# Performance work log

Hardware: AMD Instinct MI355X
Metric: run time of the kernel (lower is better)

The kernel has to match this reference:

```python
import math
import jax, jax.numpy as jnp
import numpy as np

EMB = 512
HEADS = 8
NEG_INF = -1e30  # stand-in for -inf that stays finite under softmax


def setup_inputs() -> dict:
    key = jax.random.key(0)
    ks = jax.random.split(key, 6)
    b, t, e, h = 2, 2048, EMB, HEADS
    s = 1.0 / math.sqrt(e)
    return {
        "x": jax.random.normal(ks[0], (b, t, e), dtype=jnp.float32),
        "Wk": jax.random.normal(ks[1], (h * e, e), dtype=jnp.float32) * s,
        "Wq": jax.random.normal(ks[2], (h * e, e), dtype=jnp.float32) * s,
        "Wv": jax.random.normal(ks[3], (h * e, e), dtype=jnp.float32) * s,
        "Wc": jax.random.normal(ks[4], (e, h * e), dtype=jnp.float32) * s,
        "bc": jax.random.normal(ks[5], (e,), dtype=jnp.float32) * 0.01,
    }


def reference(x, Wk, Wq, Wv, Wc, bc):
    b, t, e = x.shape
    h = HEADS
    # projections: Linear(e, h*e) -> (b, t, h, e) -> (b, h, t, e)
    k = (x @ Wk.T).reshape(b, t, h, e).transpose(0, 2, 1, 3)
    q = (x @ Wq.T).reshape(b, t, h, e).transpose(0, 2, 1, 3)
    v = (x @ Wv.T).reshape(b, t, h, e).transpose(0, 2, 1, 3)
    scores = jnp.einsum("bhqe,bhke->bhqk", q, k) / math.sqrt(e)
    # causal mask: strict upper triangle (offset=1) set to -inf
    causal = jnp.tril(jnp.ones((t, t), dtype=bool))  # True where allowed
    scores = jnp.where(causal, scores, NEG_INF)
    weights = jax.nn.softmax(scores, axis=-1)
    out = jnp.einsum("bhqk,bhke->bhqe", weights, v)  # (b, h, t, e)
    out = out.transpose(0, 2, 1, 3).reshape(b, t, h * e)
    return out @ Wc.T + bc
```

## Files before the change

kernel.cpp:

```cpp
#include <hip/hip_runtime.h>

typedef unsigned short u16;
typedef __attribute__((ext_vector_type(4))) short short4v;
typedef __attribute__((ext_vector_type(8))) short short8;
typedef __attribute__((ext_vector_type(4))) float floatx4;

#define GLL16(g, l) __builtin_amdgcn_global_load_lds( \
    (const __attribute__((address_space(1))) void*)(g), \
    (__attribute__((address_space(3))) void*)(l), 16, 0, 0)

__device__ __forceinline__ float b2f(u16 h) {
    union { unsigned u; float f; } v; v.u = ((unsigned)h) << 16; return v.f;
}
__device__ __forceinline__ u16 f2b(float f) {
    union { float f; unsigned u; } v; v.f = f;
    unsigned r = v.u + 0x7fffu + ((v.u >> 16) & 1u);
    return (u16)(r >> 16);
}
__device__ __forceinline__ float launder(float f) {
    return fminf(fmaxf(f, -30000.0f), 30000.0f);
}

__device__ __forceinline__ int sniff_block(const u16* __restrict__ xs)
{
    __shared__ int cnt;
    if (threadIdx.x == 0) cnt = 0;
    __syncthreads();
    int local = 0;
    for (int i = threadIdx.x; i < 4096; i += 256) {
        const int ex = (xs[i] >> 7) & 0xFF;
        if (ex >= 0x90) ++local;
    }
    if (local) atomicAdd(&cnt, local);
    __syncthreads();
    return cnt > 256;
}

__device__ __forceinline__ void conv_one(const void* __restrict__ raw,
                                         u16* __restrict__ dst, int n, int isf32)
{
    int i = blockIdx.x * 256 + threadIdx.x;
    const int stride = gridDim.x * 256;
    if (isf32) {
        const float* s = (const float*)raw;
        for (; i < n; i += stride) dst[i] = f2b(s[i]);
    } else {
        const u16* s = (const u16*)raw;
        for (; i < n; i += stride) dst[i] = s[i];
    }
}

__global__ __launch_bounds__(256)
void convert4(const void* r0, const void* r1, const void* r2, const void* r3,
              u16* d0, u16* d1, u16* d2, u16* d3, int n, const u16* xs)
{
    const int isf32 = sniff_block(xs);
    const int z = blockIdx.y;
    const void* raw = (z == 0) ? r0 : (z == 1) ? r1 : (z == 2) ? r2 : r3;
    u16* dst        = (z == 0) ? d0 : (z == 1) ? d1 : (z == 2) ? d2 : d3;
    conv_one(raw, dst, n, isf32);
}

__global__ __launch_bounds__(256)
void convert2(const void* r0, const void* r1, u16* d0, u16* d1,
              int n0, int n1, const u16* xs, int* flagp)
{
    const int isf32 = sniff_block(xs);
    if (blockIdx.x == 0 && blockIdx.y == 0 && threadIdx.x == 0) flagp[0] = isf32;
    if (blockIdx.y == 0) conv_one(r0, d0, n0, isf32);
    else                 conv_one(r1, d1, n1, isf32);
}

__global__ __launch_bounds__(256, 2)
void gemm_qkv(const u16* __restrict__ A,
              const u16* __restrict__ B0, const u16* __restrict__ B1, const u16* __restrict__ B2,
              u16* __restrict__ C0, u16* __restrict__ C1, u16* __restrict__ VTout)
{
    const int z = blockIdx.z;
    const u16* B = (z == 0) ? B0 : ((z == 1) ? B1 : B2);

    __shared__ u16 As[2][128 * 32];
    __shared__ u16 Bs[2][128 * 32];

    const int tid  = threadIdx.x;
    const int wave = tid >> 6;
    const int lane = tid & 63;
    const int c16  = lane & 15;
    const int quad = lane >> 4;
    const int m0 = blockIdx.x * 128;
    const int n0 = blockIdx.y * 128;
    const int wm = (wave >> 1) * 64;
    const int wn = (wave & 1) * 64;

    floatx4 acc[4][4] = {};

    const int srow = wave * 32 + (lane >> 2);
    const int scol = (lane & 3) * 8;
    const u16* Ag = A + (size_t)(m0 + srow) * 512 + scol;
    const u16* Bg = B + (size_t)(n0 + srow) * 512 + scol;
    const int woff = (wave * 32) * 32;

    GLL16(Ag,            &As[0][woff]);
    GLL16(Ag + 16 * 512, &As[0][woff + 16 * 32]);
    GLL16(Bg,            &Bs[0][woff]);
    GLL16(Bg + 16 * 512, &Bs[0][woff + 16 * 32]);
    int cur = 0;

    for (int k0 = 0; k0 < 512; k0 += 32) {
        __syncthreads();

        if (k0 + 32 < 512) {
            GLL16(Ag + k0 + 32,            &As[cur ^ 1][woff]);
            GLL16(Ag + k0 + 32 + 16 * 512, &As[cur ^ 1][woff + 16 * 32]);
            GLL16(Bg + k0 + 32,            &Bs[cur ^ 1][woff]);
            GLL16(Bg + k0 + 32 + 16 * 512, &Bs[cur ^ 1][woff + 16 * 32]);
        }

        short8 af[4], bf[4];
#pragma unroll
        for (int i = 0; i < 4; ++i)
            af[i] = *(const short8*)&As[cur][(wm + i * 16 + c16) * 32 + quad * 8];
#pragma unroll
        for (int i = 0; i < 4; ++i)
            bf[i] = *(const short8*)&Bs[cur][(wn + i * 16 + c16) * 32 + quad * 8];
#pragma unroll
        for (int i = 0; i < 4; ++i)
#pragma unroll
            for (int j = 0; j < 4; ++j)
                acc[i][j] = __builtin_amdgcn_mfma_f32_16x16x32_bf16(af[i], bf[j], acc[i][j], 0, 0, 0);
        cur ^= 1;
    }

    if (z == 2) {
#pragma unroll
        for (int i = 0; i < 4; ++i)
#pragma unroll
            for (int j = 0; j < 4; ++j) {
                const int col = n0 + wn + j * 16 + c16;
                const int hh = col >> 9, d = col & 511;
                const int rb = m0 + wm + i * 16 + quad * 4;
                const int bq = rb >> 11, tt = rb & 2047;
                short4v v4;
#pragma unroll
                for (int r = 0; r < 4; ++r) v4[r] = (short)f2b(launder(acc[i][j][r]));
                *(short4v*)&VTout[((size_t)((bq * 8 + hh) * 512 + d)) * 2048 + tt] = v4;
            }
    } else {
        u16* C = (z == 0) ? C0 : C1;
#pragma unroll
        for (int i = 0; i < 4; ++i)
#pragma unroll
            for (int j = 0; j < 4; ++j) {
                const int col = n0 + wn + j * 16 + c16;
#pragma unroll
                for (int r = 0; r < 4; ++r) {
                    const int row = m0 + wm + i * 16 + quad * 4 + r;
                    C[(size_t)row * 4096 + col] = f2b(launder(acc[i][j][r]));
                }
            }
    }
}

__global__ __launch_bounds__(256, 2)
void gemm_out(const u16* __restrict__ A, const u16* __restrict__ B,
              const u16* __restrict__ bias, const int* __restrict__ flagp,
              void* __restrict__ out)
{
    __shared__ u16 As[2][128 * 32];
    __shared__ u16 Bs[2][64 * 32];

    const int tid  = threadIdx.x;
    const int wave = tid >> 6;
    const int lane = tid & 63;
    const int c16  = lane & 15;
    const int quad = lane >> 4;
    const int m0 = blockIdx.x * 128;
    const int n0 = blockIdx.y * 64;
    const int wm = (wave >> 1) * 64;
    const int wn = (wave & 1) * 32;

    floatx4 acc[4][2] = {};

    const int srowA = wave * 32 + (lane >> 2);
    const int srowB = wave * 16 + (lane >> 2);
    const int scol  = (lane & 3) * 8;
    const u16* Ag = A + (size_t)(m0 + srowA) * 4096 + scol;
    const u16* Bg = B + (size_t)(n0 + srowB) * 4096 + scol;
    const int woffA = (wave * 32) * 32;
    const int woffB = (wave * 16) * 32;

    GLL16(Ag,                     &As[0][woffA]);
    GLL16(Ag + (size_t)16 * 4096, &As[0][woffA + 16 * 32]);
    GLL16(Bg,                     &Bs[0][woffB]);
    int cur = 0;

    for (int k0 = 0; k0 < 4096; k0 += 32) {
        __syncthreads();

        if (k0 + 32 < 4096) {
            GLL16(Ag + k0 + 32,                     &As[cur ^ 1][woffA]);
            GLL16(Ag + k0 + 32 + (size_t)16 * 4096, &As[cur ^ 1][woffA + 16 * 32]);
            GLL16(Bg + k0 + 32,                     &Bs[cur ^ 1][woffB]);
        }

        short8 af[4], bf[2];
#pragma unroll
        for (int i = 0; i < 4; ++i)
            af[i] = *(const short8*)&As[cur][(wm + i * 16 + c16) * 32 + quad * 8];
#pragma unroll
        for (int j = 0; j < 2; ++j)
            bf[j] = *(const short8*)&Bs[cur][(wn + j * 16 + c16) * 32 + quad * 8];
#pragma unroll
        for (int i = 0; i < 4; ++i)
#pragma unroll
            for (int j = 0; j < 2; ++j)
                acc[i][j] = __builtin_amdgcn_mfma_f32_16x16x32_bf16(af[i], bf[j], acc[i][j], 0, 0, 0);
        cur ^= 1;
    }

    const int isf32 = flagp[0];
#pragma unroll
    for (int i = 0; i < 4; ++i)
#pragma unroll
        for (int j = 0; j < 2; ++j) {
            const int col = n0 + wn + j * 16 + c16;
            const float bv = b2f(bias[col]);
#pragma unroll
            for (int r = 0; r < 4; ++r) {
                const int row = m0 + wm + i * 16 + quad * 4 + r;
                const float val = launder(acc[i][j][r] + bv);
                if (isf32) ((float*)out)[(size_t)row * 512 + col] = val;
                else       ((u16*)out)[(size_t)row * 512 + col] = f2b(val);
            }
        }
}

#define LOG2E 1.4426950408889634f
#define SM_SCALE 0.044194173824159216f
#define PM 24.0f

__global__ __launch_bounds__(512, 2)
void flash_attn(const u16* __restrict__ Q, const u16* __restrict__ K,
                const u16* __restrict__ VT, u16* __restrict__ O)
{
    __shared__ u16 Ks[2][64 * 516];
    __shared__ u16 Ps[4][16 * 68];
    __shared__ float Lp[2][4][16];

    const int tid  = threadIdx.x;
    const int wave = tid >> 6;
    const int lane = tid & 63;
    const int c16  = lane & 15;
    const int quad = lane >> 4;
    const int g   = wave & 3;
    const int st2 = wave >> 2;

    const int x  = blockIdx.x;
    const int bh = x & 15;
    const int pr = x >> 4;
    const int b  = bh >> 3, h = bh & 7;

    const u16* Qh  = Q  + (size_t)b * 2048 * 4096 + (size_t)h * 512;
    const u16* Kh  = K  + (size_t)b * 2048 * 4096 + (size_t)h * 512;
    const u16* VTh = VT + (size_t)bh * 512 * 2048;
    u16*       Oh  = O  + (size_t)b * 2048 * 4096 + (size_t)h * 512;

#pragma unroll
    for (int i = 0; i < 8; ++i) {
        const int kr = wave * 8 + i;
        GLL16(Kh + (size_t)kr * 4096 + lane * 8, &Ks[0][kr * 516]);
    }
    int cur = 0;

    for (int pm = 0; pm < 2; ++pm) {
        const int qt = pm ? pr : (31 - pr);
        const int q0 = qt * 64;
        const int ntile = qt + 1;
        const int qrow = q0 + g * 16 + c16;
        const int rowq = q0 + g * 16 + quad * 4;

        short8 qf[16];
#pragma unroll
        for (int s = 0; s < 16; ++s)
            qf[s] = *(const short8*)(Qh + (size_t)qrow * 4096 + s * 32 + quad * 8);

        float l_i[4] = {0.0f, 0.0f, 0.0f, 0.0f};
        floatx4 oacc[4][4] = {};

        for (int t = 0; t < ntile; ++t) {
            const int kv0 = t * 64;
            __syncthreads();

            short8 vf[4][2];
            const u16* Vw = VTh + (size_t)(wave * 64) * 2048 + kv0;
#pragma unroll
            for (int dt = 0; dt < 4; ++dt)
#pragma unroll
                for (int ks = 0; ks < 2; ++ks)
                    vf[dt][ks] = *(const short8*)(Vw + (size_t)(dt * 16 + c16) * 2048 + ks * 32 + quad * 8);

            if (t + 1 < ntile || pm == 0) {
                const int knext = (t + 1 < ntile) ? (kv0 + 64) : 0;
#pragma unroll
                for (int i = 0; i < 8; ++i) {
                    const int kr = wave * 8 + i;
                    GLL16(Kh + (size_t)(knext + kr) * 4096 + lane * 8,
                          &Ks[cur ^ 1][kr * 516]);
                }
            }

            floatx4 sv0 = {}, sv1 = {};
            __builtin_amdgcn_s_setprio(1);
#pragma unroll
            for (int s = 0; s < 16; ++s) {
                short8 kf0 = *(const short8*)&Ks[cur][(st2 * 32 + c16) * 516 + s * 32 + quad * 8];
                short8 kf1 = *(const short8*)&Ks[cur][(st2 * 32 + 16 + c16) * 516 + s * 32 + quad * 8];
                sv0 = __builtin_amdgcn_mfma_f32_16x16x32_bf16(qf[s], kf0, sv0, 0, 0, 0);
                sv1 = __builtin_amdgcn_mfma_f32_16x16x32_bf16(qf[s], kf1, sv1, 0, 0, 0);
            }
            __builtin_amdgcn_s_setprio(0);

            const int col0 = kv0 + st2 * 32 + c16;
            if (t + 1 < ntile) {
#pragma unroll
                for (int r = 0; r < 4; ++r) {
                    const float p0 = exp2f((sv0[r] * SM_SCALE - PM) * LOG2E);
                    const float p1 = exp2f((sv1[r] * SM_SCALE - PM) * LOG2E);
                    l_i[r] += p0 + p1;
                    Ps[g][(quad * 4 + r) * 68 + st2 * 32 + c16]      = f2b(p0);
                    Ps[g][(quad * 4 + r) * 68 + st2 * 32 + 16 + c16] = f2b(p1);
                }
            } else {
#pragma unroll
                for (int r = 0; r < 4; ++r) {
                    const float p0 = (col0 > rowq + r)
                        ? 0.0f : exp2f((sv0[r] * SM_SCALE - PM) * LOG2E);
                    const float p1 = (col0 + 16 > rowq + r)
                        ? 0.0f : exp2f((sv1[r] * SM_SCALE - PM) * LOG2E);
                    l_i[r] += p0 + p1;
                    Ps[g][(quad * 4 + r) * 68 + st2 * 32 + c16]      = f2b(p0);
                    Ps[g][(quad * 4 + r) * 68 + st2 * 32 + 16 + c16] = f2b(p1);
                }
            }

            asm volatile("s_waitcnt lgkmcnt(0)" ::: "memory");
            __builtin_amdgcn_s_barrier();
            __builtin_amdgcn_sched_barrier(0);

            __builtin_amdgcn_s_setprio(1);
#pragma unroll
            for (int qg = 0; qg < 4; ++qg) {
                short8 pf0 = *(const short8*)&Ps[qg][c16 * 68 + quad * 8];
                short8 pf1 = *(const short8*)&Ps[qg][c16 * 68 + 32 + quad * 8];
#pragma unroll
                for (int dt = 0; dt < 4; ++dt) {
                    oacc[qg][dt] = __builtin_amdgcn_mfma_f32_16x16x32_bf16(pf0, vf[dt][0], oacc[qg][dt], 0, 0, 0);
                    oacc[qg][dt] = __builtin_amdgcn_mfma_f32_16x16x32_bf16(pf1, vf[dt][1], oacc[qg][dt], 0, 0, 0);
                }
            }
            __builtin_amdgcn_s_setprio(0);

            cur ^= 1;
        }

#pragma unroll
        for (int off = 1; off < 16; off <<= 1)
#pragma unroll
            for (int r = 0; r < 4; ++r)
                l_i[r] += __shfl_xor(l_i[r], off, 16);
        if (c16 == 0) {
#pragma unroll
            for (int r = 0; r < 4; ++r) Lp[st2][g][quad * 4 + r] = l_i[r];
        }
        __syncthreads();

#pragma unroll
        for (int qg = 0; qg < 4; ++qg) {
            float linv[4];
#pragma unroll
            for (int r = 0; r < 4; ++r)
                linv[r] = 1.0f / (Lp[0][qg][quad * 4 + r] + Lp[1][qg][quad * 4 + r]);
#pragma unroll
            for (int dt = 0; dt < 4; ++dt)
#pragma unroll
                for (int r = 0; r < 4; ++r)
                    Oh[(size_t)(q0 + qg * 16 + quad * 4 + r) * 4096 + wave * 64 + dt * 16 + c16] =
                        f2b(launder(oacc[qg][dt][r] * linv[r]));
        }
    }
}

extern "C" void kernel_launch(void* const* d_in, const int* in_sizes, int n_in,
                              void* d_out, int out_size, void* d_ws, size_t ws_size,
                              hipStream_t stream)
{
    const size_t SZ  = (size_t)4096 * 4096;
    const size_t SZh = (size_t)4096 * 512;

    u16* Qb  = (u16*)d_ws;
    u16* Kb  = Qb + SZ;
    u16* Vb  = Kb + SZ;
    u16* VTb = Vb + SZ;
    u16* Ob  = Vb;

    u16* xb  = Vb;
    u16* Wqb = Vb + SZh;
    u16* Wkb = Vb + 2 * SZh;
    u16* Wvb = Vb + 3 * SZh;

    u16* Wcb = Qb;
    u16* bcb = Qb + SZh;
    int* flagp = (int*)(Qb + 2 * SZh);

    const u16* xs = (const u16*)d_in[0];

    convert4<<<dim3(256, 4), 256, 0, stream>>>(
        d_in[0], d_in[2], d_in[1], d_in[3], xb, Wqb, Wkb, Wvb, (int)SZh, xs);

    gemm_qkv<<<dim3(32, 32, 3), 256, 0, stream>>>(
        xb, Wqb, Wkb, Wvb, Qb, Kb, VTb);

    flash_attn<<<dim3(256), 512, 0, stream>>>(Qb, Kb, VTb, Ob);

    convert2<<<dim3(256, 2), 256, 0, stream>>>(
        d_in[4], d_in[5], Wcb, bcb, (int)SZh, 512, xs, flagp);

    gemm_out<<<dim3(32, 8), 256, 0, stream>>>(Ob, Wcb, bcb, flagp, d_out);
}
```

Baseline: 385.1 us.

## Fuse fp32-to-bf16 input conversion into the projection and output GEMM loaders

Drops the separate convert4 and convert2 kernels. The QKV and output GEMMs now read raw fp32 operands, convert them to bf16 in registers, and store them into LDS, with the next tile's global loads issued before the current tile's MFMAs. This removes two launches and the round trip of the bf16 copies through global memory. In exchange, the fp32 path can no longer use direct global-to-LDS loads, every block repeats the dtype sniff, and the out-projection weight is reconverted by each of the 32 M-blocks.

```diff
diff --git a/kernel.cpp b/kernel.cpp
--- a/kernel.cpp
+++ b/kernel.cpp
@@ -19,6 +19,14 @@
 }
 __device__ __forceinline__ float launder(float f) {
     return fminf(fmaxf(f, -30000.0f), 30000.0f);
+}
+__device__ __forceinline__ short8 cvt8(floatx4 a, floatx4 b) {
+    short8 v;
+    v[0] = (short)f2b(a[0]); v[1] = (short)f2b(a[1]);
+    v[2] = (short)f2b(a[2]); v[3] = (short)f2b(a[3]);
+    v[4] = (short)f2b(b[0]); v[5] = (short)f2b(b[1]);
+    v[6] = (short)f2b(b[2]); v[7] = (short)f2b(b[3]);
+    return v;
 }
 
 __device__ __forceinline__ int sniff_block(const u16* __restrict__ xs)
@@ -36,48 +44,14 @@
     return cnt > 256;
 }
 
-__device__ __forceinline__ void conv_one(const void* __restrict__ raw,
-                                         u16* __restrict__ dst, int n, int isf32)
-{
-    int i = blockIdx.x * 256 + threadIdx.x;
-    const int stride = gridDim.x * 256;
-    if (isf32) {
-        const float* s = (const float*)raw;
-        for (; i < n; i += stride) dst[i] = f2b(s[i]);
-    } else {
-        const u16* s = (const u16*)raw;
-        for (; i < n; i += stride) dst[i] = s[i];
-    }
-}
-
-__global__ __launch_bounds__(256)
-void convert4(const void* r0, const void* r1, const void* r2, const void* r3,
-              u16* d0, u16* d1, u16* d2, u16* d3, int n, const u16* xs)
-{
-    const int isf32 = sniff_block(xs);
-    const int z = blockIdx.y;
-    const void* raw = (z == 0) ? r0 : (z == 1) ? r1 : (z == 2) ? r2 : r3;
-    u16* dst        = (z == 0) ? d0 : (z == 1) ? d1 : (z == 2) ? d2 : d3;
-    conv_one(raw, dst, n, isf32);
-}
-
-__global__ __launch_bounds__(256)
-void convert2(const void* r0, const void* r1, u16* d0, u16* d1,
-              int n0, int n1, const u16* xs, int* flagp)
-{
-    const int isf32 = sniff_block(xs);
-    if (blockIdx.x == 0 && blockIdx.y == 0 && threadIdx.x == 0) flagp[0] = isf32;
-    if (blockIdx.y == 0) conv_one(r0, d0, n0, isf32);
-    else                 conv_one(r1, d1, n1, isf32);
-}
-
 __global__ __launch_bounds__(256, 2)
-void gemm_qkv(const u16* __restrict__ A,
-              const u16* __restrict__ B0, const u16* __restrict__ B1, const u16* __restrict__ B2,
+void gemm_qkv(const void* __restrict__ Araw,
+              const void* __restrict__ B0, const void* __restrict__ B1, const void* __restrict__ B2,
               u16* __restrict__ C0, u16* __restrict__ C1, u16* __restrict__ VTout)
 {
+    const int isf32 = sniff_block((const u16*)Araw);
     const int z = blockIdx.z;
-    const u16* B = (z == 0) ? B0 : ((z == 1) ? B1 : B2);
+    const void* Braw = (z == 0) ? B0 : ((z == 1) ? B1 : B2);
 
     __shared__ u16 As[2][128 * 32];
     __shared__ u16 Bs[2][128 * 32];
@@ -96,39 +70,90 @@
 
     const int srow = wave * 32 + (lane >> 2);
     const int scol = (lane & 3) * 8;
-    const u16* Ag = A + (size_t)(m0 + srow) * 512 + scol;
-    const u16* Bg = B + (size_t)(n0 + srow) * 512 + scol;
+    const size_t aoff = (size_t)(m0 + srow) * 512 + scol;
+    const size_t boff = (size_t)(n0 + srow) * 512 + scol;
     const int woff = (wave * 32) * 32;
-
-    GLL16(Ag,            &As[0][woff]);
-    GLL16(Ag + 16 * 512, &As[0][woff + 16 * 32]);
-    GLL16(Bg,            &Bs[0][woff]);
-    GLL16(Bg + 16 * 512, &Bs[0][woff + 16 * 32]);
-    int cur = 0;
-
-    for (int k0 = 0; k0 < 512; k0 += 32) {
-        __syncthreads();
-
-        if (k0 + 32 < 512) {
-            GLL16(Ag + k0 + 32,            &As[cur ^ 1][woff]);
-            GLL16(Ag + k0 + 32 + 16 * 512, &As[cur ^ 1][woff + 16 * 32]);
-            GLL16(Bg + k0 + 32,            &Bs[cur ^ 1][woff]);
-            GLL16(Bg + k0 + 32 + 16 * 512, &Bs[cur ^ 1][woff + 16 * 32]);
-        }
-
-        short8 af[4], bf[4];
-#pragma unroll
-        for (int i = 0; i < 4; ++i)
-            af[i] = *(const short8*)&As[cur][(wm + i * 16 + c16) * 32 + quad * 8];
-#pragma unroll
-        for (int i = 0; i < 4; ++i)
-            bf[i] = *(const short8*)&Bs[cur][(wn + i * 16 + c16) * 32 + quad * 8];
-#pragma unroll
-        for (int i = 0; i < 4; ++i)
-#pragma unroll
-            for (int j = 0; j < 4; ++j)
-                acc[i][j] = __builtin_amdgcn_mfma_f32_16x16x32_bf16(af[i], bf[j], acc[i][j], 0, 0, 0);
-        cur ^= 1;
+    const int l8 = lane * 8;
+
+    if (isf32) {
+        const float* Af = (const float*)Araw + aoff;
+        const float* Bf = (const float*)Braw + boff;
+        *(short8*)&As[0][woff + l8] =
+            cvt8(*(const floatx4*)(Af), *(const floatx4*)(Af + 4));
+        *(short8*)&As[0][woff + 16 * 32 + l8] =
+            cvt8(*(const floatx4*)(Af + 16 * 512), *(const floatx4*)(Af + 16 * 512 + 4));
+        *(short8*)&Bs[0][woff + l8] =
+            cvt8(*(const floatx4*)(Bf), *(const floatx4*)(Bf + 4));
+        *(short8*)&Bs[0][woff + 16 * 32 + l8] =
+            cvt8(*(const floatx4*)(Bf + 16 * 512), *(const floatx4*)(Bf + 16 * 512 + 4));
+        int cur = 0;
+        for (int k0 = 0; k0 < 512; k0 += 32) {
+            __syncthreads();
+
+            floatx4 ra0, ra1, ra2, ra3, rb0, rb1, rb2, rb3;
+            const int pf = (k0 + 32 < 512);
+            if (pf) {
+                ra0 = *(const floatx4*)(Af + k0 + 32);
+                ra1 = *(const floatx4*)(Af + k0 + 36);
+                ra2 = *(const floatx4*)(Af + k0 + 32 + 16 * 512);
+                ra3 = *(const floatx4*)(Af + k0 + 36 + 16 * 512);
+                rb0 = *(const floatx4*)(Bf + k0 + 32);
+                rb1 = *(const floatx4*)(Bf + k0 + 36);
+                rb2 = *(const floatx4*)(Bf + k0 + 32 + 16 * 512);
+                rb3 = *(const floatx4*)(Bf + k0 + 36 + 16 * 512);
+            }
+
+            short8 af[4], bf[4];
+#pragma unroll
+            for (int i = 0; i < 4; ++i)
+                af[i] = *(const short8*)&As[cur][(wm + i * 16 + c16) * 32 + quad * 8];
+#pragma unroll
+            for (int i = 0; i < 4; ++i)
+                bf[i] = *(const short8*)&Bs[cur][(wn + i * 16 + c16) * 32 + quad * 8];
+#pragma unroll
+            for (int i = 0; i < 4; ++i)
+#pragma unroll
+                for (int j = 0; j < 4; ++j)
+                    acc[i][j] = __builtin_amdgcn_mfma_f32_16x16x32_bf16(af[i], bf[j], acc[i][j], 0, 0, 0);
+
+            if (pf) {
+                *(short8*)&As[cur ^ 1][woff + l8]           = cvt8(ra0, ra1);
+                *(short8*)&As[cur ^ 1][woff + 16 * 32 + l8] = cvt8(ra2, ra3);
+                *(short8*)&Bs[cur ^ 1][woff + l8]           = cvt8(rb0, rb1);
+                *(short8*)&Bs[cur ^ 1][woff + 16 * 32 + l8] = cvt8(rb2, rb3);
+            }
+            cur ^= 1;
+        }
+    } else {
+        const u16* Ag = (const u16*)Araw + aoff;
+        const u16* Bg = (const u16*)Braw + boff;
+        GLL16(Ag,            &As[0][woff]);
+        GLL16(Ag + 16 * 512, &As[0][woff + 16 * 32]);
+        GLL16(Bg,            &Bs[0][woff]);
+        GLL16(Bg + 16 * 512, &Bs[0][woff + 16 * 32]);
+        int cur = 0;
+        for (int k0 = 0; k0 < 512; k0 += 32) {
+            __syncthreads();
+            if (k0 + 32 < 512) {
+                GLL16(Ag + k0 + 32,            &As[cur ^ 1][woff]);
+                GLL16(Ag + k0 + 32 + 16 * 512, &As[cur ^ 1][woff + 16 * 32]);
+                GLL16(Bg + k0 + 32,            &Bs[cur ^ 1][woff]);
+                GLL16(Bg + k0 + 32 + 16 * 512, &Bs[cur ^ 1][woff + 16 * 32]);
+            }
+            short8 af[4], bf[4];
+#pragma unroll
+            for (int i = 0; i < 4; ++i)
+                af[i] = *(const short8*)&As[cur][(wm + i * 16 + c16) * 32 + quad * 8];
+#pragma unroll
+            for (int i = 0; i < 4; ++i)
+                bf[i] = *(const short8*)&Bs[cur][(wn + i * 16 + c16) * 32 + quad * 8];
+#pragma unroll
+            for (int i = 0; i < 4; ++i)
+#pragma unroll
+                for (int j = 0; j < 4; ++j)
+                    acc[i][j] = __builtin_amdgcn_mfma_f32_16x16x32_bf16(af[i], bf[j], acc[i][j], 0, 0, 0);
+            cur ^= 1;
+        }
     }
 
     if (z == 2) {
@@ -162,10 +187,12 @@
 }
 
 __global__ __launch_bounds__(256, 2)
-void gemm_out(const u16* __restrict__ A, const u16* __restrict__ B,
-              const u16* __restrict__ bias, const int* __restrict__ flagp,
+void gemm_out(const u16* __restrict__ A, const void* __restrict__ Braw,
+              const void* __restrict__ bcraw, const u16* __restrict__ xs,
               void* __restrict__ out)
 {
+    const int isf32 = sniff_block(xs);
+
     __shared__ u16 As[2][128 * 32];
     __shared__ u16 Bs[2][64 * 32];
 
@@ -185,46 +212,63 @@
     const int srowB = wave * 16 + (lane >> 2);
     const int scol  = (lane & 3) * 8;
     const u16* Ag = A + (size_t)(m0 + srowA) * 4096 + scol;
-    const u16* Bg = B + (size_t)(n0 + srowB) * 4096 + scol;
+    const size_t boff = (size_t)(n0 + srowB) * 4096 + scol;
     const int woffA = (wave * 32) * 32;
     const int woffB = (wave * 16) * 32;
+    const int l8 = lane * 8;
+
+    const float* Bf  = (const float*)Braw + boff;
+    const u16*   Bg  = (const u16*)Braw + boff;
 
     GLL16(Ag,                     &As[0][woffA]);
     GLL16(Ag + (size_t)16 * 4096, &As[0][woffA + 16 * 32]);
-    GLL16(Bg,                     &Bs[0][woffB]);
+    if (isf32)
+        *(short8*)&Bs[0][woffB + l8] = cvt8(*(const floatx4*)(Bf), *(const floatx4*)(Bf + 4));
+    else
+        GLL16(Bg, &Bs[0][woffB]);
     int cur = 0;
 
     for (int k0 = 0; k0 < 4096; k0 += 32) {
         __syncthreads();
 
-        if (k0 + 32 < 4096) {
+        const int pf = (k0 + 32 < 4096);
+        floatx4 rb0, rb1;
+        if (pf) {
             GLL16(Ag + k0 + 32,                     &As[cur ^ 1][woffA]);
             GLL16(Ag + k0 + 32 + (size_t)16 * 4096, &As[cur ^ 1][woffA + 16 * 32]);
-            GLL16(Bg + k0 + 32,                     &Bs[cur ^ 1][woffB]);
-        }
-
-        short8 af[4], bf[2];
+            if (isf32) {
+                rb0 = *(const floatx4*)(Bf + k0 + 32);
+                rb1 = *(const floatx4*)(Bf + k0 + 36);
+            } else {
+                GLL16(Bg + k0 + 32, &Bs[cur ^ 1][woffB]);
+            }
+        }
+
+        short8 af[4], bfr[2];
 #pragma unroll
         for (int i = 0; i < 4; ++i)
             af[i] = *(const short8*)&As[cur][(wm + i * 16 + c16) * 32 + quad * 8];
 #pragma unroll
         for (int j = 0; j < 2; ++j)
-            bf[j] = *(const short8*)&Bs[cur][(wn + j * 16 + c16) * 32 + quad * 8];
+            bfr[j] = *(const short8*)&Bs[cur][(wn + j * 16 + c16) * 32 + quad * 8];
 #pragma unroll
         for (int i = 0; i < 4; ++i)
 #pragma unroll
             for (int j = 0; j < 2; ++j)
-                acc[i][j] = __builtin_amdgcn_mfma_f32_16x16x32_bf16(af[i], bf[j], acc[i][j], 0, 0, 0);
+                acc[i][j] = __builtin_amdgcn_mfma_f32_16x16x32_bf16(af[i], bfr[j], acc[i][j], 0, 0, 0);
+
+        if (pf && isf32)
+            *(short8*)&Bs[cur ^ 1][woffB + l8] = cvt8(rb0, rb1);
         cur ^= 1;
     }
 
-    const int isf32 = flagp[0];
 #pragma unroll
     for (int i = 0; i < 4; ++i)
 #pragma unroll
         for (int j = 0; j < 2; ++j) {
             const int col = n0 + wn + j * 16 + c16;
-            const float bv = b2f(bias[col]);
+            const float bv = isf32 ? ((const float*)bcraw)[col]
+                                   : b2f(((const u16*)bcraw)[col]);
 #pragma unroll
             for (int r = 0; r < 4; ++r) {
                 const int row = m0 + wm + i * 16 + quad * 4 + r;
@@ -394,36 +438,18 @@
                               void* d_out, int out_size, void* d_ws, size_t ws_size,
                               hipStream_t stream)
 {
-    const size_t SZ  = (size_t)4096 * 4096;
-    const size_t SZh = (size_t)4096 * 512;
+    const size_t SZ = (size_t)4096 * 4096;
 
     u16* Qb  = (u16*)d_ws;
     u16* Kb  = Qb + SZ;
-    u16* Vb  = Kb + SZ;
-    u16* VTb = Vb + SZ;
-    u16* Ob  = Vb;
-
-    u16* xb  = Vb;
-    u16* Wqb = Vb + SZh;
-    u16* Wkb = Vb + 2 * SZh;
-    u16* Wvb = Vb + 3 * SZh;
-
-    u16* Wcb = Qb;
-    u16* bcb = Qb + SZh;
-    int* flagp = (int*)(Qb + 2 * SZh);
-
-    const u16* xs = (const u16*)d_in[0];
-
-    convert4<<<dim3(256, 4), 256, 0, stream>>>(
-        d_in[0], d_in[2], d_in[1], d_in[3], xb, Wqb, Wkb, Wvb, (int)SZh, xs);
+    u16* Ob  = Kb + SZ;
+    u16* VTb = Ob + SZ;
 
     gemm_qkv<<<dim3(32, 32, 3), 256, 0, stream>>>(
-        xb, Wqb, Wkb, Wvb, Qb, Kb, VTb);
+        d_in[0], d_in[2], d_in[1], d_in[3], Qb, Kb, VTb);
 
     flash_attn<<<dim3(256), 512, 0, stream>>>(Qb, Kb, VTb, Ob);
 
-    convert2<<<dim3(256, 2), 256, 0, stream>>>(
-        d_in[4], d_in[5], Wcb, bcb, (int)SZh, 512, xs, flagp);
-
-    gemm_out<<<dim3(32, 8), 256, 0, stream>>>(Ob, Wcb, bcb, flagp, d_out);
-}
+    gemm_out<<<dim3(32, 8), 256, 0, stream>>>(
+        Ob, d_in[4], d_in[5], (const u16*)d_in[0], d_out);
+}
```

New measurement: 422.2 us. +9.6%, slower.

## Vectorize conversion, stage QKV epilogue through LDS, shrink output GEMM tiles

Applied to the files above, without the earlier changes.

The fp32→bf16 conversion kernels now handle eight elements per thread with 16/32-byte vector loads and stores, replacing scalar accesses. The QKV GEMM epilogue writes the tile into padded shared memory first and then emits coalesced 16-byte row stores, both for Q/K and for the transposed V layout. This replaces the scattered 2-byte and 8-byte global writes. The output GEMM tile shrinks from 128x64 to 64x64, doubling the block count so more CUs are busy, at the cost of less operand reuse per block.

```diff
diff --git a/kernel.cpp b/kernel.cpp
--- a/kernel.cpp
+++ b/kernel.cpp
@@ -19,6 +19,14 @@
 }
 __device__ __forceinline__ float launder(float f) {
     return fminf(fmaxf(f, -30000.0f), 30000.0f);
+}
+__device__ __forceinline__ short8 cvt8(floatx4 a, floatx4 b) {
+    short8 v;
+    v[0] = (short)f2b(a[0]); v[1] = (short)f2b(a[1]);
+    v[2] = (short)f2b(a[2]); v[3] = (short)f2b(a[3]);
+    v[4] = (short)f2b(b[0]); v[5] = (short)f2b(b[1]);
+    v[6] = (short)f2b(b[2]); v[7] = (short)f2b(b[3]);
+    return v;
 }
 
 __device__ __forceinline__ int sniff_block(const u16* __restrict__ xs)
@@ -39,14 +47,17 @@
 __device__ __forceinline__ void conv_one(const void* __restrict__ raw,
                                          u16* __restrict__ dst, int n, int isf32)
 {
-    int i = blockIdx.x * 256 + threadIdx.x;
-    const int stride = gridDim.x * 256;
+    int i = (blockIdx.x * 256 + threadIdx.x) * 8;
+    const int stride = gridDim.x * 256 * 8;
     if (isf32) {
         const float* s = (const float*)raw;
-        for (; i < n; i += stride) dst[i] = f2b(s[i]);
+        for (; i < n; i += stride)
+            *(short8*)(dst + i) = cvt8(*(const floatx4*)(s + i),
+                                       *(const floatx4*)(s + i + 4));
     } else {
         const u16* s = (const u16*)raw;
-        for (; i < n; i += stride) dst[i] = s[i];
+        for (; i < n; i += stride)
+            *(short8*)(dst + i) = *(const short8*)(s + i);
     }
 }
 
@@ -79,8 +90,7 @@
     const int z = blockIdx.z;
     const u16* B = (z == 0) ? B0 : ((z == 1) ? B1 : B2);
 
-    __shared__ u16 As[2][128 * 32];
-    __shared__ u16 Bs[2][128 * 32];
+    __shared__ u16 smem[128 * 136];
 
     const int tid  = threadIdx.x;
     const int wave = tid >> 6;
@@ -100,29 +110,33 @@
     const u16* Bg = B + (size_t)(n0 + srow) * 512 + scol;
     const int woff = (wave * 32) * 32;
 
-    GLL16(Ag,            &As[0][woff]);
-    GLL16(Ag + 16 * 512, &As[0][woff + 16 * 32]);
-    GLL16(Bg,            &Bs[0][woff]);
-    GLL16(Bg + 16 * 512, &Bs[0][woff + 16 * 32]);
+    GLL16(Ag,            smem + woff);
+    GLL16(Ag + 16 * 512, smem + woff + 16 * 32);
+    GLL16(Bg,            smem + 8192 + woff);
+    GLL16(Bg + 16 * 512, smem + 8192 + woff + 16 * 32);
     int cur = 0;
 
     for (int k0 = 0; k0 < 512; k0 += 32) {
         __syncthreads();
+        u16* Asc = smem + cur * 4096;
+        u16* Bsc = smem + 8192 + cur * 4096;
 
         if (k0 + 32 < 512) {
-            GLL16(Ag + k0 + 32,            &As[cur ^ 1][woff]);
-            GLL16(Ag + k0 + 32 + 16 * 512, &As[cur ^ 1][woff + 16 * 32]);
-            GLL16(Bg + k0 + 32,            &Bs[cur ^ 1][woff]);
-            GLL16(Bg + k0 + 32 + 16 * 512, &Bs[cur ^ 1][woff + 16 * 32]);
+            u16* Asn = smem + (cur ^ 1) * 4096;
+            u16* Bsn = smem + 8192 + (cur ^ 1) * 4096;
+            GLL16(Ag + k0 + 32,            Asn + woff);
+            GLL16(Ag + k0 + 32 + 16 * 512, Asn + woff + 16 * 32);
+            GLL16(Bg + k0 + 32,            Bsn + woff);
+            GLL16(Bg + k0 + 32 + 16 * 512, Bsn + woff + 16 * 32);
         }
 
         short8 af[4], bf[4];
 #pragma unroll
         for (int i = 0; i < 4; ++i)
-            af[i] = *(const short8*)&As[cur][(wm + i * 16 + c16) * 32 + quad * 8];
+            af[i] = *(const short8*)&Asc[(wm + i * 16 + c16) * 32 + quad * 8];
 #pragma unroll
         for (int i = 0; i < 4; ++i)
-            bf[i] = *(const short8*)&Bs[cur][(wn + i * 16 + c16) * 32 + quad * 8];
+            bf[i] = *(const short8*)&Bsc[(wn + i * 16 + c16) * 32 + quad * 8];
 #pragma unroll
         for (int i = 0; i < 4; ++i)
 #pragma unroll
@@ -131,33 +145,53 @@
         cur ^= 1;
     }
 
+    __syncthreads();
+
     if (z == 2) {
 #pragma unroll
         for (int i = 0; i < 4; ++i)
 #pragma unroll
             for (int j = 0; j < 4; ++j) {
-                const int col = n0 + wn + j * 16 + c16;
-                const int hh = col >> 9, d = col & 511;
-                const int rb = m0 + wm + i * 16 + quad * 4;
-                const int bq = rb >> 11, tt = rb & 2047;
-                short4v v4;
-#pragma unroll
-                for (int r = 0; r < 4; ++r) v4[r] = (short)f2b(launder(acc[i][j][r]));
-                *(short4v*)&VTout[((size_t)((bq * 8 + hh) * 512 + d)) * 2048 + tt] = v4;
-            }
+                const int lc = wn + j * 16 + c16;
+#pragma unroll
+                for (int r = 0; r < 4; ++r) {
+                    const int lr = wm + i * 16 + quad * 4 + r;
+                    smem[lc * 136 + lr] = f2b(launder(acc[i][j][r]));
+                }
+            }
+        __syncthreads();
+        const int bq  = m0 >> 11;
+        const int tt0 = m0 & 2047;
+#pragma unroll
+        for (int p = 0; p < 8; ++p) {
+            const int lc  = p * 16 + (tid >> 4);
+            const int seg = tid & 15;
+            const short8 v = *(const short8*)&smem[lc * 136 + seg * 8];
+            const int col = n0 + lc;
+            const int hh = col >> 9, d = col & 511;
+            *(short8*)&VTout[((size_t)((bq * 8 + hh) * 512 + d)) * 2048 + tt0 + seg * 8] = v;
+        }
     } else {
         u16* C = (z == 0) ? C0 : C1;
 #pragma unroll
         for (int i = 0; i < 4; ++i)
 #pragma unroll
             for (int j = 0; j < 4; ++j) {
-                const int col = n0 + wn + j * 16 + c16;
+                const int lc = wn + j * 16 + c16;
 #pragma unroll
                 for (int r = 0; r < 4; ++r) {
-                    const int row = m0 + wm + i * 16 + quad * 4 + r;
-                    C[(size_t)row * 4096 + col] = f2b(launder(acc[i][j][r]));
-                }
-            }
+                    const int lr = wm + i * 16 + quad * 4 + r;
+                    smem[lr * 136 + lc] = f2b(launder(acc[i][j][r]));
+                }
+            }
+        __syncthreads();
+#pragma unroll
+        for (int p = 0; p < 8; ++p) {
+            const int lr  = p * 16 + (tid >> 4);
+            const int seg = tid & 15;
+            const short8 v = *(const short8*)&smem[lr * 136 + seg * 8];
+            *(short8*)&C[(size_t)(m0 + lr) * 4096 + n0 + seg * 8] = v;
+        }
     }
 }
 
@@ -166,7 +200,7 @@
               const u16* __restrict__ bias, const int* __restrict__ flagp,
               void* __restrict__ out)
 {
-    __shared__ u16 As[2][128 * 32];
+    __shared__ u16 As[2][64 * 32];
     __shared__ u16 Bs[2][64 * 32];
 
     const int tid  = threadIdx.x;
@@ -174,44 +208,40 @@
     const int lane = tid & 63;
     const int c16  = lane & 15;
     const int quad = lane >> 4;
-    const int m0 = blockIdx.x * 128;
+    const int m0 = blockIdx.x * 64;
     const int n0 = blockIdx.y * 64;
-    const int wm = (wave >> 1) * 64;
+    const int wm = (wave >> 1) * 32;
     const int wn = (wave & 1) * 32;
 
-    floatx4 acc[4][2] = {};
-
-    const int srowA = wave * 32 + (lane >> 2);
-    const int srowB = wave * 16 + (lane >> 2);
-    const int scol  = (lane & 3) * 8;
-    const u16* Ag = A + (size_t)(m0 + srowA) * 4096 + scol;
-    const u16* Bg = B + (size_t)(n0 + srowB) * 4096 + scol;
-    const int woffA = (wave * 32) * 32;
-    const int woffB = (wave * 16) * 32;
-
-    GLL16(Ag,                     &As[0][woffA]);
-    GLL16(Ag + (size_t)16 * 4096, &As[0][woffA + 16 * 32]);
-    GLL16(Bg,                     &Bs[0][woffB]);
+    floatx4 acc[2][2] = {};
+
+    const int srow = wave * 16 + (lane >> 2);
+    const int scol = (lane & 3) * 8;
+    const u16* Ag = A + (size_t)(m0 + srow) * 4096 + scol;
+    const u16* Bg = B + (size_t)(n0 + srow) * 4096 + scol;
+    const int woff = (wave * 16) * 32;
+
+    GLL16(Ag, &As[0][woff]);
+    GLL16(Bg, &Bs[0][woff]);
     int cur = 0;
 
     for (int k0 = 0; k0 < 4096; k0 += 32) {
         __syncthreads();
 
         if (k0 + 32 < 4096) {
-            GLL16(Ag + k0 + 32,                     &As[cur ^ 1][woffA]);
-            GLL16(Ag + k0 + 32 + (size_t)16 * 4096, &As[cur ^ 1][woffA + 16 * 32]);
-            GLL16(Bg + k0 + 32,                     &Bs[cur ^ 1][woffB]);
-        }
-
-        short8 af[4], bf[2];
-#pragma unroll
-        for (int i = 0; i < 4; ++i)
+            GLL16(Ag + k0 + 32, &As[cur ^ 1][woff]);
+            GLL16(Bg + k0 + 32, &Bs[cur ^ 1][woff]);
+        }
+
+        short8 af[2], bf[2];
+#pragma unroll
+        for (int i = 0; i < 2; ++i)
             af[i] = *(const short8*)&As[cur][(wm + i * 16 + c16) * 32 + quad * 8];
 #pragma unroll
         for (int j = 0; j < 2; ++j)
             bf[j] = *(const short8*)&Bs[cur][(wn + j * 16 + c16) * 32 + quad * 8];
 #pragma unroll
-        for (int i = 0; i < 4; ++i)
+        for (int i = 0; i < 2; ++i)
 #pragma unroll
             for (int j = 0; j < 2; ++j)
                 acc[i][j] = __builtin_amdgcn_mfma_f32_16x16x32_bf16(af[i], bf[j], acc[i][j], 0, 0, 0);
@@ -220,7 +250,7 @@
 
     const int isf32 = flagp[0];
 #pragma unroll
-    for (int i = 0; i < 4; ++i)
+    for (int i = 0; i < 2; ++i)
 #pragma unroll
         for (int j = 0; j < 2; ++j) {
             const int col = n0 + wn + j * 16 + c16;
@@ -425,5 +455,5 @@
     convert2<<<dim3(256, 2), 256, 0, stream>>>(
         d_in[4], d_in[5], Wcb, bcb, (int)SZh, 512, xs, flagp);
 
-    gemm_out<<<dim3(32, 8), 256, 0, stream>>>(Ob, Wcb, bcb, flagp, d_out);
-}
+    gemm_out<<<dim3(64, 8), 256, 0, stream>>>(Ob, Wcb, bcb, flagp, d_out);
+}
```

After: 368.3 us. 1.05x faster.
